# Performance work log

Measured on AMD Instinct MI355X. Metric: run time of the kernel, lower is better.

The kernel has to match this reference:

```python
import jax, jax.numpy as jnp
import numpy as np

# ---- constants derived from init_kwargs (level_i=0) ----
STRIDE = 8
BASE = 4 * STRIDE  # cfg['model.retina.anchor.base'] * stride = 32
SCALES = [1.0, 1.2599, 1.5874]
RATIOS = [[1.0, 1.0], [1.4, 0.7], [0.7, 1.4]]
ANCHOR_WH = jnp.asarray([[BASE * s * r[0], BASE * s * r[1]] for s in SCALES for r in RATIOS],
                        dtype=jnp.float32)  # [nA, 2]
POS_THRES = 0.5
NEG_THRES = 0.4
NCLS = 80


def _anchor_boxes(nA, nH, nW):
    """Anchor boxes in cxcywh, shape [nA, nH, nW, 4] (cx varies over W, cy over H, wh over A)."""
    a_cx = (jnp.arange(nW, dtype=jnp.float32) + 0.5) * STRIDE  # [nW]
    a_cy = (jnp.arange(nH, dtype=jnp.float32) + 0.5) * STRIDE  # [nH]
    cx = jnp.broadcast_to(a_cx[None, None, :, None], (nA, nH, nW, 1))
    cy = jnp.broadcast_to(a_cy[None, :, None, None], (nA, nH, nW, 1))
    wh = jnp.broadcast_to(ANCHOR_WH[:, None, None, :], (nA, nH, nW, 2))
    return jnp.concatenate([cx, cy, wh], axis=-1)


def _iou_cxcywh(anch, gt):
    """anch: [N,4] cxcywh, gt: [B,G,4] cxcywh -> iou [B,N,G]."""
    a_tl = anch[:, :2] - anch[:, 2:] * 0.5  # [N,2]
    a_br = anch[:, :2] + anch[:, 2:] * 0.5
    g_tl = gt[..., :2] - gt[..., 2:] * 0.5  # [B,G,2]
    g_br = gt[..., :2] + gt[..., 2:] * 0.5
    tl = jnp.maximum(a_tl[None, :, None, :], g_tl[:, None, :, :])  # [B,N,G,2]
    br = jnp.minimum(a_br[None, :, None, :], g_br[:, None, :, :])
    inter = jnp.prod(jnp.clip(br - tl, 0.0, None), axis=-1)  # [B,N,G]
    area_a = anch[:, 2] * anch[:, 3]          # [N]
    area_g = gt[..., 2] * gt[..., 3]          # [B,G]
    union = area_a[None, :, None] + area_g[:, None, :] - inter
    return inter / union


def setup_inputs() -> dict:
    key = jax.random.key(0)
    k1, k2, k3, k4, k5 = jax.random.split(key, 5)
    B, nA, nH, nW, nGT = 8, 9, 64, 64, 32
    t_xywh = jax.random.normal(k1, (B, nA, nH, nW, 4), dtype=jnp.float32) * 0.1
    cls_logits = jax.random.normal(k2, (B, nA, nH, nW, NCLS), dtype=jnp.float32)
    # GT boxes (cx, cy, w, h), valid inside a 512x512 image
    cxy = jax.random.uniform(k3, (B, nGT, 2), minval=32.0, maxval=480.0, dtype=jnp.float32)
    wh = jax.random.uniform(k4, (B, nGT, 2), minval=16.0, maxval=160.0, dtype=jnp.float32)
    gt_bboxes = jnp.concatenate([cxy, wh], axis=-1)
    gt_cats = jax.random.randint(k5, (B, nGT), 0, NCLS)
    return {"t_xywh": t_xywh, "cls_logits": cls_logits, "gt_bboxes": gt_bboxes,
            "gt_cats": gt_cats, "img_h": 512, "img_w": 512}


def reference(t_xywh, cls_logits, gt_bboxes, gt_cats, img_h, img_w):
    B, nA, nH, nW, _ = t_xywh.shape
    nCls = cls_logits.shape[-1]
    N = nA * nH * nW

    anch = _anchor_boxes(nA, nH, nW).reshape(N, 4)  # [N,4]

    ious = _iou_cxcywh(anch, gt_bboxes)             # [B,N,G]
    iou_with_gt = jnp.max(ious, axis=-1)            # [B,N]
    gt_idx = jnp.argmax(ious, axis=-1)              # [B,N]

    pos = iou_with_gt > POS_THRES                   # [B,N]
    neg = iou_with_gt < NEG_THRES
    penalty = pos | neg

    # gather matched GT box / category per anchor
    gb = jnp.take_along_axis(gt_bboxes, gt_idx[:, :, None], axis=1)  # [B,N,4]
    gc = jnp.take_along_axis(gt_cats, gt_idx, axis=1)                # [B,N]

    tgt_xy = (gb[..., :2] - anch[None, :, :2]) / anch[None, :, 2:]
    tgt_wh = jnp.log(gb[..., 2:] / anch[None, :, 2:] + 1e-8)
    tgt_xywh = jnp.concatenate([tgt_xy, tgt_wh], axis=-1)            # [B,N,4]

    t_flat = t_xywh.reshape(B, N, 4)
    posf = pos.astype(t_flat.dtype)
    loss_xywh = jnp.sum(posf[..., None] * (t_flat - tgt_xywh) ** 2)

    # class targets: one-hot at positive anchors, zeros elsewhere
    tgt_cls = jax.nn.one_hot(gc, nCls, dtype=t_flat.dtype) * posf[..., None]  # [B,N,C]
    x = cls_logits.reshape(B, N, nCls)
    # stable BCE-with-logits, summed per image over penalty anchors
    bce = jnp.maximum(x, 0.0) - x * tgt_cls + jnp.log1p(jnp.exp(-jnp.abs(x)))
    penf = penalty.astype(x.dtype)
    im_loss_cls = jnp.sum(penf[..., None] * bce, axis=(1, 2))   # [B]
    num_pos = jnp.sum(posf, axis=1)                             # [B]
    loss_cls = jnp.sum(im_loss_cls / (num_pos + 1.0))

    loss = (loss_xywh + loss_cls) / B
    return loss
```

## Files before the change

kernel.cpp:

```cpp
#include <hip/hip_runtime.h>

#define NCLS   80
#define NB     8
#define NGT    32
#define NANCH  36864
#define BLK_A  128
#define NTHR   256
#define NBLK   2304
#define BLKS_PER_IMG 288
#define KI     10

#define LOG2E 1.4426950408889634f
#define LN2   0.6931471805599453f

__device__ __constant__ float c_aw[9] = {
    (float)(32.0 * 1.0    * 1.0), (float)(32.0 * 1.0    * 1.4), (float)(32.0 * 1.0    * 0.7),
    (float)(32.0 * 1.2599 * 1.0), (float)(32.0 * 1.2599 * 1.4), (float)(32.0 * 1.2599 * 0.7),
    (float)(32.0 * 1.5874 * 1.0), (float)(32.0 * 1.5874 * 1.4), (float)(32.0 * 1.5874 * 0.7)};
__device__ __constant__ float c_ah[9] = {
    (float)(32.0 * 1.0    * 1.0), (float)(32.0 * 1.0    * 0.7), (float)(32.0 * 1.0    * 1.4),
    (float)(32.0 * 1.2599 * 1.0), (float)(32.0 * 1.2599 * 0.7), (float)(32.0 * 1.2599 * 1.4),
    (float)(32.0 * 1.5874 * 1.0), (float)(32.0 * 1.5874 * 0.7), (float)(32.0 * 1.5874 * 1.4)};

__global__ __launch_bounds__(NTHR, 8) void retina_main(
    const float* __restrict__ t_xywh,
    const float* __restrict__ cls_logits,
    const float* __restrict__ gt_bboxes,
    const int*   __restrict__ gt_cats,
    float4* __restrict__ part)
{
    __shared__ float s_best[NTHR];
    __shared__ int   s_bi[NTHR];
    __shared__ int   s_flag[BLK_A];
    __shared__ float s_red[4 * 3];

    const int tid = threadIdx.x;
    const int blk = blockIdx.x;
    const int b   = blk / BLKS_PER_IMG;
    const int la0 = tid & (BLK_A - 1);
    const int gh  = tid >> 7;

    const int n  = (blk % BLKS_PER_IMG) * BLK_A + la0;
    const int a  = n >> 12;
    const int hy = (n >> 6) & 63;
    const int wx = n & 63;
    const float acx = (wx + 0.5f) * 8.0f;
    const float acy = (hy + 0.5f) * 8.0f;
    const float aw  = c_aw[a];
    const float ah  = c_ah[a];

    const float4* gt4  = (const float4*)gt_bboxes + b * NGT;
    const int*    gcat = gt_cats + b * NGT;

    float best = -1.0f;
    int   bi   = 0;
    {
        const float a_tlx = acx - aw * 0.5f, a_tly = acy - ah * 0.5f;
        const float a_brx = acx + aw * 0.5f, a_bry = acy + ah * 0.5f;
        const float area_a = aw * ah;
        const int g0 = gh * 16;
        for (int j = 0; j < 16; ++j) {
            const int gg = g0 + j;
            const float4 gb = gt4[gg];
            const float g_tlx = gb.x - gb.z * 0.5f, g_tly = gb.y - gb.w * 0.5f;
            const float g_brx = gb.x + gb.z * 0.5f, g_bry = gb.y + gb.w * 0.5f;
            float dx = fminf(a_brx, g_brx) - fmaxf(a_tlx, g_tlx);
            float dy = fminf(a_bry, g_bry) - fmaxf(a_tly, g_tly);
            dx = fmaxf(dx, 0.0f);
            dy = fmaxf(dy, 0.0f);
            const float inter = dx * dy;
            const float uni   = area_a + gb.z * gb.w - inter;
            const float iou   = inter * __builtin_amdgcn_rcpf(uni);
            if (iou > best) { best = iou; bi = gg; }
        }
    }
    s_best[tid] = best;
    s_bi[tid]   = bi;
    __syncthreads();

    float lx = 0.0f, pcnt = 0.0f;
    if (tid < BLK_A) {
        const float bhi = s_best[tid + BLK_A];
        if (bhi > best) { best = bhi; bi = s_bi[tid + BLK_A]; }
        const bool pos = best > 0.5f;
        const bool neg = best < 0.4f;
        int f = (pos | neg) ? 256 : -1;
        if (pos) {
            f    = gcat[bi];
            pcnt = 1.0f;
            const float4 g = gt4[bi];
            const float4 t = ((const float4*)t_xywh)[(size_t)b * NANCH + n];
            const float tx = (g.x - acx) / aw;
            const float ty = (g.y - acy) / ah;
            const float tw = logf(g.z / aw + 1e-8f);
            const float th = logf(g.w / ah + 1e-8f);
            const float d0 = t.x - tx, d1 = t.y - ty, d2 = t.z - tw, d3 = t.w - th;
            lx = d0 * d0 + d1 * d1 + d2 * d2 + d3 * d3;
        }
        s_flag[tid] = f;
    }
    __syncthreads();

    const float4* base = (const float4*)cls_logits + (size_t)blk * (BLK_A * NCLS / 4);
    float l2 = 0.0f, hot = 0.0f;
#pragma unroll
    for (int k = 0; k < KI; ++k) {
        const int e  = k * NTHR + tid;
        const int la = e / 20;
        const float4 x = base[e];
        const int fl = s_flag[la];
        const float t0 = __builtin_amdgcn_exp2f(x.x * LOG2E);
        const float t1 = __builtin_amdgcn_exp2f(x.y * LOG2E);
        const float t2 = __builtin_amdgcn_exp2f(x.z * LOG2E);
        const float t3 = __builtin_amdgcn_exp2f(x.w * LOG2E);
        const float g0 = __builtin_amdgcn_logf(1.0f + t0);
        const float g1 = __builtin_amdgcn_logf(1.0f + t1);
        const float g2 = __builtin_amdgcn_logf(1.0f + t2);
        const float g3 = __builtin_amdgcn_logf(1.0f + t3);
        const float m  = (fl >= 0) ? 1.0f : 0.0f;
        l2 += m * ((g0 + g1) + (g2 + g3));
        if (__any((unsigned)fl < NCLS)) {
            const int c0 = (e - la * 20) * 4;
            hot += (fl == c0    ) ? x.x : 0.0f;
            hot += (fl == c0 + 1) ? x.y : 0.0f;
            hot += (fl == c0 + 2) ? x.z : 0.0f;
            hot += (fl == c0 + 3) ? x.w : 0.0f;
        }
    }
    const float lc = LN2 * l2 - hot;

    float v0 = lc, v1 = lx, v2 = pcnt;
    for (int o = 32; o > 0; o >>= 1) {
        v0 += __shfl_down(v0, o);
        v1 += __shfl_down(v1, o);
        v2 += __shfl_down(v2, o);
    }
    const int wave = tid >> 6;
    if ((tid & 63) == 0) {
        s_red[wave * 3 + 0] = v0;
        s_red[wave * 3 + 1] = v1;
        s_red[wave * 3 + 2] = v2;
    }
    __syncthreads();
    if (tid == 0) {
        float c = 0.0f, xw = 0.0f, pc = 0.0f;
        for (int w2 = 0; w2 < 4; ++w2) {
            c  += s_red[w2 * 3 + 0];
            xw += s_red[w2 * 3 + 1];
            pc += s_red[w2 * 3 + 2];
        }
        part[blk] = make_float4(c, xw, pc, 0.0f);
    }
}

__global__ __launch_bounds__(256) void retina_final(
    const float4* __restrict__ part, float* __restrict__ out)
{
    __shared__ float s_lc[NB], s_pc[NB], s_lx[NB];
    const int tid = threadIdx.x;
    const int b = tid >> 5, l = tid & 31;

    float lc = 0.0f, lx = 0.0f, pc = 0.0f;
    for (int i = l; i < BLKS_PER_IMG; i += 32) {
        const float4 p = part[b * BLKS_PER_IMG + i];
        lc += p.x; lx += p.y; pc += p.z;
    }
    for (int o = 16; o > 0; o >>= 1) {
        lc += __shfl_xor(lc, o);
        lx += __shfl_xor(lx, o);
        pc += __shfl_xor(pc, o);
    }
    if (l == 0) { s_lc[b] = lc; s_pc[b] = pc; s_lx[b] = lx; }
    __syncthreads();

    if (tid == 0) {
        float s = 0.0f, lxt = 0.0f;
        for (int bb = 0; bb < NB; ++bb) {
            lxt += s_lx[bb];
            s   += s_lc[bb] / (s_pc[bb] + 1.0f);
        }
        out[0] = (lxt + s) / (float)NB;
    }
}

extern "C" void kernel_launch(void* const* d_in, const int* in_sizes, int n_in,
                              void* d_out, int out_size, void* d_ws, size_t ws_size,
                              hipStream_t stream)
{
    const float* t_xywh     = (const float*)d_in[0];
    const float* cls_logits = (const float*)d_in[1];
    const float* gt_bboxes  = (const float*)d_in[2];
    const int*   gt_cats    = (const int*)d_in[3];

    float4* part = (float4*)d_ws;

    retina_main<<<NBLK, NTHR, 0, stream>>>(t_xywh, cls_logits, gt_bboxes, gt_cats, part);
    retina_final<<<1, 256, 0, stream>>>(part, (float*)d_out);
}
```

Before: 27.69 us.

## Fuse final reduction via last-block atomic counter and precompute GT corners in LDS

The separate final reduction kernel is folded into the main kernel: each block publishes its partial sums, then increments a global counter, and the last block to finish reduces all partials and writes the loss. GT box corners, areas and categories are precomputed once per block into shared memory. The one-hot logit is now fetched directly for positive anchors, which removes the per-element category compare from the streaming loop. In exchange, a memset of the counter is added before launch, along with a threadfence and atomic per block.

```diff
diff --git a/kernel.cpp b/kernel.cpp
--- a/kernel.cpp
+++ b/kernel.cpp
@@ -4,7 +4,7 @@
 #define NB     8
 #define NGT    32
 #define NANCH  36864
-#define BLK_A  128
+#define APB    128
 #define NTHR   256
 #define NBLK   2304
 #define BLKS_PER_IMG 288
@@ -27,20 +27,41 @@
     const float* __restrict__ cls_logits,
     const float* __restrict__ gt_bboxes,
     const int*   __restrict__ gt_cats,
-    float4* __restrict__ part)
+    float4* __restrict__ part,
+    unsigned int* __restrict__ counter,
+    float* __restrict__ out)
 {
-    __shared__ float s_best[NTHR];
-    __shared__ int   s_bi[NTHR];
-    __shared__ int   s_flag[BLK_A];
-    __shared__ float s_red[4 * 3];
+    __shared__ float4 s_gtl[NGT];
+    __shared__ float  s_ga[NGT];
+    __shared__ int    s_cat[NGT];
+    __shared__ float  s_best[NTHR];
+    __shared__ int    s_bi[NTHR];
+    __shared__ float  s_mask[APB];
+    __shared__ float  s_red[4 * 4];
+    __shared__ int    s_last;
 
     const int tid = threadIdx.x;
     const int blk = blockIdx.x;
     const int b   = blk / BLKS_PER_IMG;
-    const int la0 = tid & (BLK_A - 1);
+    const int la0 = tid & (APB - 1);
     const int gh  = tid >> 7;
 
-    const int n  = (blk % BLKS_PER_IMG) * BLK_A + la0;
+    const float4* gt4  = (const float4*)gt_bboxes + b * NGT;
+    const int*    gcat = gt_cats + b * NGT;
+
+    {
+#pragma clang fp contract(off)
+        if (tid < NGT) {
+            const float4 gb = gt4[tid];
+            s_gtl[tid] = make_float4(gb.x - gb.z * 0.5f, gb.y - gb.w * 0.5f,
+                                     gb.x + gb.z * 0.5f, gb.y + gb.w * 0.5f);
+            s_ga[tid]  = gb.z * gb.w;
+            s_cat[tid] = gcat[tid];
+        }
+    }
+    __syncthreads();
+
+    const int n  = (blk % BLKS_PER_IMG) * APB + la0;
     const int a  = n >> 12;
     const int hy = (n >> 6) & 63;
     const int wx = n & 63;
@@ -49,27 +70,23 @@
     const float aw  = c_aw[a];
     const float ah  = c_ah[a];
 
-    const float4* gt4  = (const float4*)gt_bboxes + b * NGT;
-    const int*    gcat = gt_cats + b * NGT;
-
     float best = -1.0f;
     int   bi   = 0;
     {
+#pragma clang fp contract(off)
         const float a_tlx = acx - aw * 0.5f, a_tly = acy - ah * 0.5f;
         const float a_brx = acx + aw * 0.5f, a_bry = acy + ah * 0.5f;
         const float area_a = aw * ah;
         const int g0 = gh * 16;
         for (int j = 0; j < 16; ++j) {
             const int gg = g0 + j;
-            const float4 gb = gt4[gg];
-            const float g_tlx = gb.x - gb.z * 0.5f, g_tly = gb.y - gb.w * 0.5f;
-            const float g_brx = gb.x + gb.z * 0.5f, g_bry = gb.y + gb.w * 0.5f;
-            float dx = fminf(a_brx, g_brx) - fmaxf(a_tlx, g_tlx);
-            float dy = fminf(a_bry, g_bry) - fmaxf(a_tly, g_tly);
+            const float4 e4 = s_gtl[gg];
+            float dx = fminf(a_brx, e4.z) - fmaxf(a_tlx, e4.x);
+            float dy = fminf(a_bry, e4.w) - fmaxf(a_tly, e4.y);
             dx = fmaxf(dx, 0.0f);
             dy = fmaxf(dy, 0.0f);
             const float inter = dx * dy;
-            const float uni   = area_a + gb.z * gb.w - inter;
+            const float uni   = (area_a + s_ga[gg]) - inter;
             const float iou   = inter * __builtin_amdgcn_rcpf(uni);
             if (iou > best) { best = iou; bi = gg; }
         }
@@ -78,16 +95,16 @@
     s_bi[tid]   = bi;
     __syncthreads();
 
-    float lx = 0.0f, pcnt = 0.0f;
-    if (tid < BLK_A) {
-        const float bhi = s_best[tid + BLK_A];
-        if (bhi > best) { best = bhi; bi = s_bi[tid + BLK_A]; }
+    float lx = 0.0f, pcnt = 0.0f, hot = 0.0f;
+    if (tid < APB) {
+        const float bhi = s_best[tid + APB];
+        if (bhi > best) { best = bhi; bi = s_bi[tid + APB]; }
         const bool pos = best > 0.5f;
         const bool neg = best < 0.4f;
-        int f = (pos | neg) ? 256 : -1;
         if (pos) {
-            f    = gcat[bi];
+            const int cat = s_cat[bi];
             pcnt = 1.0f;
+            hot  = cls_logits[((size_t)blk * APB + tid) * NCLS + cat];
             const float4 g = gt4[bi];
             const float4 t = ((const float4*)t_xywh)[(size_t)b * NANCH + n];
             const float tx = (g.x - acx) / aw;
@@ -97,18 +114,18 @@
             const float d0 = t.x - tx, d1 = t.y - ty, d2 = t.z - tw, d3 = t.w - th;
             lx = d0 * d0 + d1 * d1 + d2 * d2 + d3 * d3;
         }
-        s_flag[tid] = f;
-    }
-    __syncthreads();
-
-    const float4* base = (const float4*)cls_logits + (size_t)blk * (BLK_A * NCLS / 4);
-    float l2 = 0.0f, hot = 0.0f;
+        s_mask[tid] = (pos | neg) ? 1.0f : 0.0f;
+    }
+    __syncthreads();
+
+    const float4* base = (const float4*)cls_logits + (size_t)blk * (APB * NCLS / 4);
+    float l2 = 0.0f;
 #pragma unroll
     for (int k = 0; k < KI; ++k) {
         const int e  = k * NTHR + tid;
         const int la = e / 20;
         const float4 x = base[e];
-        const int fl = s_flag[la];
+        const float m  = s_mask[la];
         const float t0 = __builtin_amdgcn_exp2f(x.x * LOG2E);
         const float t1 = __builtin_amdgcn_exp2f(x.y * LOG2E);
         const float t2 = __builtin_amdgcn_exp2f(x.z * LOG2E);
@@ -117,69 +134,65 @@
         const float g1 = __builtin_amdgcn_logf(1.0f + t1);
         const float g2 = __builtin_amdgcn_logf(1.0f + t2);
         const float g3 = __builtin_amdgcn_logf(1.0f + t3);
-        const float m  = (fl >= 0) ? 1.0f : 0.0f;
         l2 += m * ((g0 + g1) + (g2 + g3));
-        if (__any((unsigned)fl < NCLS)) {
-            const int c0 = (e - la * 20) * 4;
-            hot += (fl == c0    ) ? x.x : 0.0f;
-            hot += (fl == c0 + 1) ? x.y : 0.0f;
-            hot += (fl == c0 + 2) ? x.z : 0.0f;
-            hot += (fl == c0 + 3) ? x.w : 0.0f;
-        }
-    }
-    const float lc = LN2 * l2 - hot;
-
-    float v0 = lc, v1 = lx, v2 = pcnt;
+    }
+
+    float v0 = l2, v1 = lx, v2 = pcnt, v3 = hot;
     for (int o = 32; o > 0; o >>= 1) {
         v0 += __shfl_down(v0, o);
         v1 += __shfl_down(v1, o);
         v2 += __shfl_down(v2, o);
+        v3 += __shfl_down(v3, o);
     }
     const int wave = tid >> 6;
     if ((tid & 63) == 0) {
-        s_red[wave * 3 + 0] = v0;
-        s_red[wave * 3 + 1] = v1;
-        s_red[wave * 3 + 2] = v2;
+        s_red[wave * 4 + 0] = v0;
+        s_red[wave * 4 + 1] = v1;
+        s_red[wave * 4 + 2] = v2;
+        s_red[wave * 4 + 3] = v3;
     }
     __syncthreads();
     if (tid == 0) {
-        float c = 0.0f, xw = 0.0f, pc = 0.0f;
+        float q0 = 0.0f, q1 = 0.0f, q2 = 0.0f, q3 = 0.0f;
         for (int w2 = 0; w2 < 4; ++w2) {
-            c  += s_red[w2 * 3 + 0];
-            xw += s_red[w2 * 3 + 1];
-            pc += s_red[w2 * 3 + 2];
-        }
-        part[blk] = make_float4(c, xw, pc, 0.0f);
-    }
-}
-
-__global__ __launch_bounds__(256) void retina_final(
-    const float4* __restrict__ part, float* __restrict__ out)
-{
-    __shared__ float s_lc[NB], s_pc[NB], s_lx[NB];
-    const int tid = threadIdx.x;
-    const int b = tid >> 5, l = tid & 31;
-
-    float lc = 0.0f, lx = 0.0f, pc = 0.0f;
-    for (int i = l; i < BLKS_PER_IMG; i += 32) {
-        const float4 p = part[b * BLKS_PER_IMG + i];
-        lc += p.x; lx += p.y; pc += p.z;
-    }
-    for (int o = 16; o > 0; o >>= 1) {
-        lc += __shfl_xor(lc, o);
-        lx += __shfl_xor(lx, o);
-        pc += __shfl_xor(pc, o);
-    }
-    if (l == 0) { s_lc[b] = lc; s_pc[b] = pc; s_lx[b] = lx; }
-    __syncthreads();
-
-    if (tid == 0) {
-        float s = 0.0f, lxt = 0.0f;
-        for (int bb = 0; bb < NB; ++bb) {
-            lxt += s_lx[bb];
-            s   += s_lc[bb] / (s_pc[bb] + 1.0f);
-        }
-        out[0] = (lxt + s) / (float)NB;
+            q0 += s_red[w2 * 4 + 0];
+            q1 += s_red[w2 * 4 + 1];
+            q2 += s_red[w2 * 4 + 2];
+            q3 += s_red[w2 * 4 + 3];
+        }
+        part[blk] = make_float4(q0, q1, q2, q3);
+        __threadfence();
+        const unsigned old = atomicAdd(counter, 1u);
+        s_last = (old == NBLK - 1) ? 1 : 0;
+    }
+    __syncthreads();
+
+    if (s_last) {
+        __threadfence();
+        __shared__ float s_l2[NB], s_pc[NB], s_ht[NB], s_lxr[NB];
+        const int img = tid >> 5, l = tid & 31;
+        float l2s = 0.0f, lxs = 0.0f, pcs = 0.0f, hts = 0.0f;
+        for (int i = l; i < BLKS_PER_IMG; i += 32) {
+            const float4 p = part[img * BLKS_PER_IMG + i];
+            l2s += p.x; lxs += p.y; pcs += p.z; hts += p.w;
+        }
+        for (int o = 16; o > 0; o >>= 1) {
+            l2s += __shfl_xor(l2s, o);
+            lxs += __shfl_xor(lxs, o);
+            pcs += __shfl_xor(pcs, o);
+            hts += __shfl_xor(hts, o);
+        }
+        if (l == 0) { s_l2[img] = l2s; s_pc[img] = pcs; s_ht[img] = hts; s_lxr[img] = lxs; }
+        __syncthreads();
+        if (tid == 0) {
+            float s = 0.0f, lxt = 0.0f;
+            for (int bb = 0; bb < NB; ++bb) {
+                lxt += s_lxr[bb];
+                const float lc_b = LN2 * s_l2[bb] - s_ht[bb];
+                s += lc_b / (s_pc[bb] + 1.0f);
+            }
+            out[0] = (lxt + s) / (float)NB;
+        }
     }
 }
 
@@ -193,7 +206,9 @@
     const int*   gt_cats    = (const int*)d_in[3];
 
     float4* part = (float4*)d_ws;
-
-    retina_main<<<NBLK, NTHR, 0, stream>>>(t_xywh, cls_logits, gt_bboxes, gt_cats, part);
-    retina_final<<<1, 256, 0, stream>>>(part, (float*)d_out);
+    unsigned int* counter = (unsigned int*)((char*)d_ws + NBLK * sizeof(float4));
+
+    hipMemsetAsync(counter, 0, sizeof(unsigned int), stream);
+    retina_main<<<NBLK, NTHR, 0, stream>>>(t_xywh, cls_logits, gt_bboxes, gt_cats,
+                                           part, counter, (float*)d_out);
 }
```

Result: slower. 102.5 us (+270.2%).
